# Kernel optimization log

Hardware: AMD Instinct MI355X
Metric: run time of the kernel (lower is better)

## Reference

```python
import jax, jax.numpy as jnp
import numpy as np

N_FACTORS = 4
N_ITERATIONS = 2
N_LAYERS = 1
DEG_EPS = 1e-8
L2_EPS = 1e-12


def _l2norm(x):
    # torch F.normalize(p=2, dim=1): x / max(||x||, eps)
    n = jnp.sqrt(jnp.sum(x * x, axis=-1, keepdims=True))
    return x / jnp.maximum(n, L2_EPS)


def setup_inputs() -> dict:
    key = jax.random.key(0)
    k1, k2, k3, k4, k5, k6, k7 = jax.random.split(key, 7)
    n_users, n_items, D, M, B = 40000, 20000, 128, 600000, 4096
    return {
        "user_emb": jax.random.normal(k1, (n_users, D), dtype=jnp.float32) * 0.02,
        "item_emb": jax.random.normal(k2, (n_items, D), dtype=jnp.float32) * 0.02,
        "row": jax.random.randint(k3, (M,), 0, n_users, dtype=jnp.int32),
        "col": jax.random.randint(k4, (M,), 0, n_items, dtype=jnp.int32),
        "users": jax.random.randint(k5, (B,), 0, n_users, dtype=jnp.int32),
        "pos": jax.random.randint(k6, (B,), 0, n_items, dtype=jnp.int32),
        "neg": jax.random.randint(k7, (B,), 0, n_items, dtype=jnp.int32),
    }


def reference(user_emb, item_emb, row, col, users, pos, neg):
    n_users = user_emb.shape[0]
    n_nodes = n_users + item_emb.shape[0]
    D = user_emb.shape[1]
    d = D // N_FACTORS

    # symmetric edge list: (u -> i+offset) and (i+offset -> u)
    h = jnp.concatenate([row, col + n_users])  # [E]
    t = jnp.concatenate([col + n_users, row])  # [E]
    E = h.shape[0]

    ego = jnp.concatenate([user_emb, item_emb], axis=0)  # [N, D]
    A = jnp.ones((E, N_FACTORS), dtype=ego.dtype)
    all_emb = [ego]

    for _layer in range(N_LAYERS):
        ego_f = ego.reshape(n_nodes, N_FACTORS, d)  # factor chunks
        factor_emb = None
        for it in range(N_ITERATIONS):
            # build_matrix: per-factor edge softmax + D^-0.5 A D^-0.5
            norm_A = jax.nn.softmax(A, axis=1)                         # [E, F]
            deg = jax.ops.segment_sum(norm_A, h, num_segments=n_nodes)  # [N, F]
            deg = 1.0 / jnp.sqrt(jnp.maximum(deg, DEG_EPS))
            edge_w = norm_A * deg[h] * deg[t]                          # [E, F]
            # per-factor sparse spmm: gather tail, weight, scatter to head
            edge_val = ego_f[t] * edge_w[:, :, None]                   # [E, F, d]
            factor_emb = jax.ops.segment_sum(edge_val, h, num_segments=n_nodes)  # [N, F, d]
            if it < N_ITERATIONS - 1:
                # routing score update (final update is unused by forward)
                hn = _l2norm(factor_emb[h])   # [E, F, d]
                tn = _l2norm(ego_f[t])        # [E, F, d]
                A = A + jnp.sum(hn * jnp.tanh(tn), axis=-1)
        ego = factor_emb.reshape(n_nodes, D)
        all_emb.append(ego)

    out = jnp.mean(jnp.stack(all_emb, axis=1), axis=1)  # [N, D]
    u_g = out[:n_users]
    i_g = out[n_users:]
    return u_g[users], i_g[pos], i_g[neg]
```

## Files before the change

### kernel.cpp

```cpp
#include <hip/hip_runtime.h>
#include <hip/hip_fp16.h>
#include <math.h>

#define NU 40000
#define NI 20000
#define NN 60000
#define DD 128
#define NF 4
#define ME 600000
#define NE 1200000
#define NB 4096
#define NBLK 235
#define CPAD 16


__device__ __forceinline__ const float* node_row(const float* ue, const float* ie, int n) {
    return (n < NU) ? (ue + (size_t)n * DD) : (ie + (size_t)(n - NU) * DD);
}

typedef _Float16 hf2_t __attribute__((ext_vector_type(2)));
__device__ __forceinline__ float fdot2f(unsigned int a, unsigned int b, float c) {
#if __has_builtin(__builtin_amdgcn_fdot2)
    return __builtin_amdgcn_fdot2(__builtin_bit_cast(hf2_t, a),
                                  __builtin_bit_cast(hf2_t, b), c, false);
#else
    float2 fa = __half22float2(__builtin_bit_cast(__half2, a));
    float2 fb = __half22float2(__builtin_bit_cast(__half2, b));
    return c + fa.x * fb.x + fa.y * fb.y;
#endif
}


__global__ void k_zero(int* counts, unsigned char* flags) {
    int i = blockIdx.x * blockDim.x + threadIdx.x;
    if (i < NN * CPAD) counts[i] = 0;
    if (i < NN) flags[i] = 0;
}

__global__ void k_flag(const int* __restrict__ users, const int* __restrict__ pos,
                       const int* __restrict__ neg, unsigned char* __restrict__ flags) {
    int i = blockIdx.x * blockDim.x + threadIdx.x;
    if (i >= 3 * NB) return;
    int which = i >> 12, k = i & 4095;
    int n = (which == 0) ? users[k] : ((which == 1) ? NU + pos[k] : NU + neg[k]);
    flags[n] = 1;
}

__global__ void k_count(const int* __restrict__ row, const int* __restrict__ col,
                        int* __restrict__ counts, int* __restrict__ rank) {
    int base = (blockIdx.x * blockDim.x + threadIdx.x) * 4;
    if (base >= NE) return;
    int4 h4;
    if (base < ME) {
        h4 = *(const int4*)(row + base);
    } else {
        int4 c4 = *(const int4*)(col + (base - ME));
        h4 = make_int4(NU + c4.x, NU + c4.y, NU + c4.z, NU + c4.w);
    }
    int4 r;
    r.x = atomicAdd(&counts[h4.x * CPAD], 1);
    r.y = atomicAdd(&counts[h4.y * CPAD], 1);
    r.z = atomicAdd(&counts[h4.z * CPAD], 1);
    r.w = atomicAdd(&counts[h4.w * CPAD], 1);
    *(int4*)(rank + base) = r;
}


__global__ void k_scanA(const int* __restrict__ counts, int* __restrict__ pre,
                        int* __restrict__ bsum) {
    int tid = threadIdx.x;
    int i = blockIdx.x * 256 + tid;
    int v = (i < NN) ? counts[i * CPAD] : 0;
    int lane = tid & 63, w = tid >> 6;
    int s = v;
    #pragma unroll
    for (int off = 1; off < 64; off <<= 1) {
        int o = __shfl_up(s, off);
        if (lane >= off) s += o;
    }
    __shared__ int wsum[4];
    if (lane == 63) wsum[w] = s;
    __syncthreads();
    int add = 0;
    #pragma unroll
    for (int k = 0; k < 4; ++k) add += (k < w) ? wsum[k] : 0;
    if (i < NN) pre[i] = s - v + add;
    if (tid == 255) bsum[blockIdx.x] = add + s;
}

__global__ void k_scanB(const int* __restrict__ bsum, int* __restrict__ boff) {
    int tid = threadIdx.x;
    int v = (tid < NBLK) ? bsum[tid] : 0;
    int lane = tid & 63, w = tid >> 6;
    int s = v;
    #pragma unroll
    for (int off = 1; off < 64; off <<= 1) {
        int o = __shfl_up(s, off);
        if (lane >= off) s += o;
    }
    __shared__ int wsum[4];
    if (lane == 63) wsum[w] = s;
    __syncthreads();
    int add = 0;
    #pragma unroll
    for (int k = 0; k < 4; ++k) add += (k < w) ? wsum[k] : 0;
    if (tid < NBLK) boff[tid] = s - v + add;
}

__global__ void k_scanC(const int* __restrict__ pre, const int* __restrict__ boff,
                        const int* __restrict__ counts,
                        int* __restrict__ row_ptr, float* __restrict__ dinv0) {
    int i = blockIdx.x * 256 + threadIdx.x;
    if (i < NN) {
        row_ptr[i] = pre[i] + boff[blockIdx.x];
        dinv0[i]   = 1.0f / sqrtf(fmaxf(0.25f * (float)counts[i * CPAD], 1e-8f));
    }
    if (i == 0) row_ptr[NN] = NE;
}

__global__ void k_fill(const int* __restrict__ row, const int* __restrict__ col,
                       const int* __restrict__ row_ptr, const int* __restrict__ rank,
                       unsigned short* __restrict__ t_sorted) {
    int base = (blockIdx.x * blockDim.x + threadIdx.x) * 4;
    if (base >= NE) return;
    int4 h4, t4;
    if (base < ME) {
        h4 = *(const int4*)(row + base);
        int4 c4 = *(const int4*)(col + base);
        t4 = make_int4(NU + c4.x, NU + c4.y, NU + c4.z, NU + c4.w);
    } else {
        int4 c4 = *(const int4*)(col + (base - ME));
        h4 = make_int4(NU + c4.x, NU + c4.y, NU + c4.z, NU + c4.w);
        t4 = *(const int4*)(row + (base - ME));
    }
    int4 r = *(const int4*)(rank + base);
    t_sorted[row_ptr[h4.x] + r.x] = (unsigned short)t4.x;
    t_sorted[row_ptr[h4.y] + r.y] = (unsigned short)t4.y;
    t_sorted[row_ptr[h4.z] + r.z] = (unsigned short)t4.z;
    t_sorted[row_ptr[h4.w] + r.w] = (unsigned short)t4.w;
}

__global__ void k_prep(const float* __restrict__ ue, const float* __restrict__ ie,
                       const float* __restrict__ dinv0,
                       __half* __restrict__ ego16s, __half* __restrict__ ttan) {
    int i = blockIdx.x * blockDim.x + threadIdx.x;
    if (i >= NN * 16) return;
    int n = i >> 4;
    int il = i & 15;
    const float* src = node_row(ue, ie, n) + il * 8;
    float4 a = *(const float4*)src;
    float4 b = *(const float4*)(src + 4);
    float w = dinv0[n];
    __half2 h[4] = { __floats2half2_rn(w * a.x, w * a.y), __floats2half2_rn(w * a.z, w * a.w),
                     __floats2half2_rn(w * b.x, w * b.y), __floats2half2_rn(w * b.z, w * b.w) };
    ((float4*)ego16s)[i] = *(float4*)h;
    float s2 = a.x * a.x + a.y * a.y + a.z * a.z + a.w * a.w
             + b.x * b.x + b.y * b.y + b.z * b.z + b.w * b.w;
    s2 += __shfl_xor(s2, 1); s2 += __shfl_xor(s2, 2);
    float inv = 1.0f / fmaxf(sqrtf(s2), 1e-12f);
    __half2 t[4] = { __floats2half2_rn(tanhf(a.x * inv), tanhf(a.y * inv)),
                     __floats2half2_rn(tanhf(a.z * inv), tanhf(a.w * inv)),
                     __floats2half2_rn(tanhf(b.x * inv), tanhf(b.y * inv)),
                     __floats2half2_rn(tanhf(b.z * inv), tanhf(b.w * inv)) };
    ((float4*)ttan)[i] = *(float4*)t;
}

__global__ void k_mega(const int* __restrict__ row_ptr,
                       const unsigned short* __restrict__ t_sorted,
                       const __half* __restrict__ ego16s, const __half* __restrict__ ttan,
                       const unsigned char* __restrict__ flags,
                       float* __restrict__ normA, float* __restrict__ dinv1) {
    int n = blockIdx.x * 4 + (threadIdx.x >> 6);
    if (n >= NN) return;
    int lane = threadIdx.x & 63;
    int p0 = row_ptr[n], p1 = row_ptr[n + 1];
    bool writeA = flags[n] != 0;

    int g2 = lane >> 5;
    int jl = lane & 31;
    float4 acc = make_float4(0.f, 0.f, 0.f, 0.f);
    #pragma unroll 4
    for (int pb = p0; pb < p1; pb += 2) {
        int p = pb + g2;
        bool valid = p < p1;
        int pc = valid ? p : (p1 - 1);
        float m = valid ? 1.0f : 0.0f;
        int t = t_sorted[pc];
        float2 raw = ((const float2*)(ego16s + (size_t)t * DD))[jl];
        float2 v01 = __half22float2(*(const __half2*)&raw.x);
        float2 v23 = __half22float2(*(const __half2*)&raw.y);
        acc.x += m * v01.x; acc.y += m * v01.y;
        acc.z += m * v23.x; acc.w += m * v23.y;
    }
    acc.x += __shfl_xor(acc.x, 32); acc.y += __shfl_xor(acc.y, 32);
    acc.z += __shfl_xor(acc.z, 32); acc.w += __shfl_xor(acc.w, 32);
    float ss = acc.x * acc.x + acc.y * acc.y + acc.z * acc.z + acc.w * acc.w;
    ss += __shfl_xor(ss, 1); ss += __shfl_xor(ss, 2); ss += __shfl_xor(ss, 4);
    float inv = 1.0f / fmaxf(sqrtf(ss), 1e-12f);
    unsigned int u01 = __builtin_bit_cast(unsigned int,
                         __floats2half2_rn(acc.x * inv, acc.y * inv));
    unsigned int u23 = __builtin_bit_cast(unsigned int,
                         __floats2half2_rn(acc.z * inv, acc.w * inv));
    int il = lane & 15;
    uint4 au;
    au.x = __shfl(u01, 2 * il);
    au.y = __shfl(u23, 2 * il);
    au.z = __shfl(u01, 2 * il + 1);
    au.w = __shfl(u23, 2 * il + 1);

    int g = lane >> 4;
    int f = il >> 2;
    float dacc = 0.0f;
    #pragma unroll 4
    for (int pb = p0; pb < p1; pb += 4) {
        int p = pb + g;
        bool valid = p < p1;
        int pc = valid ? p : (p1 - 1);
        int t = t_sorted[pc];
        uint4 bu = ((const uint4*)(ttan + (size_t)t * DD))[il];
        float s = 0.0f;
        s = fdot2f(au.x, bu.x, s);
        s = fdot2f(au.y, bu.y, s);
        s = fdot2f(au.z, bu.z, s);
        s = fdot2f(au.w, bu.w, s);
        s += __shfl_xor(s, 1);
        s += __shfl_xor(s, 2);
        float m1 = fmaxf(s, __shfl_xor(s, 4));
        float mx = fmaxf(m1, __shfl_xor(m1, 8));
        float e = __expf(s - mx);
        float sum = e;
        sum += __shfl_xor(sum, 4);
        sum += __shfl_xor(sum, 8);
        float v = e * __builtin_amdgcn_rcpf(sum);
        if (valid) {
            if (writeA && (il & 3) == 0) normA[(size_t)pc * 4 + f] = v;
            dacc += v;
        }
    }
    dacc += __shfl_xor(dacc, 16);
    dacc += __shfl_xor(dacc, 32);
    if (g == 0 && (il & 3) == 0)
        dinv1[(size_t)n * 4 + f] = 1.0f / sqrtf(fmaxf(dacc, 1e-8f));
}

__global__ void k_prop1_out(const float* __restrict__ ue, const float* __restrict__ ie,
                            const int* __restrict__ row_ptr,
                            const unsigned short* __restrict__ t_sorted,
                            const float* __restrict__ normA, const float* __restrict__ dinv1,
                            const int* __restrict__ users, const int* __restrict__ pos,
                            const int* __restrict__ neg, float* __restrict__ out) {
    int r = blockIdx.x * 8 + (threadIdx.x >> 5);
    if (r >= 3 * NB) return;
    int j = threadIdx.x & 31;
    int f = j >> 3;
    int which = r >> 12;
    int i = r & 4095;
    int n;
    if (which == 0)      n = users[i];
    else if (which == 1) n = NU + pos[i];
    else                 n = NU + neg[i];
    int p0 = row_ptr[n], p1 = row_ptr[n + 1];
    float4 acc = make_float4(0.f, 0.f, 0.f, 0.f);
    #pragma unroll 4
    for (int p = p0; p < p1; ++p) {
        int t = t_sorted[p];
        float w = normA[(size_t)p * 4 + f] * dinv1[(size_t)t * 4 + f];
        float4 v = ((const float4*)node_row(ue, ie, t))[j];
        acc.x += w * v.x; acc.y += w * v.y;
        acc.z += w * v.z; acc.w += w * v.w;
    }
    float dn = dinv1[(size_t)n * 4 + f];
    float4 e0 = ((const float4*)node_row(ue, ie, n))[j];
    ((float4*)(out + (size_t)r * DD))[j] =
        make_float4(0.5f * (e0.x + dn * acc.x), 0.5f * (e0.y + dn * acc.y),
                    0.5f * (e0.z + dn * acc.z), 0.5f * (e0.w + dn * acc.w));
}


extern "C" void kernel_launch(void* const* d_in, const int* in_sizes, int n_in,
                              void* d_out, int out_size, void* d_ws, size_t ws_size,
                              hipStream_t stream) {
    const float* ue   = (const float*)d_in[0];
    const float* ie   = (const float*)d_in[1];
    const int* row    = (const int*)d_in[2];
    const int* col    = (const int*)d_in[3];
    const int* users  = (const int*)d_in[4];
    const int* pos    = (const int*)d_in[5];
    const int* neg    = (const int*)d_in[6];
    float* out        = (float*)d_out;

    char* ws = (char*)d_ws;
    size_t off = 0;
    auto take = [&](size_t bytes) { void* p = ws + off; off += (bytes + 255) & ~(size_t)255; return p; };
    __half* ttan     = (__half*)take((size_t)NN * DD * 2);
    __half* ego16s   = (__half*)take((size_t)NN * DD * 2);
    float*  normA    = (float*)take((size_t)NE * 4 * 4);
    float*  dinv1    = (float*)take((size_t)NN * 4 * 4);
    float*  dinv0    = (float*)take((size_t)NN * 4);
    int*    row_ptr  = (int*)take((size_t)(NN + 1) * 4);
    int*    counts   = (int*)take((size_t)NN * CPAD * 4);
    int*    pre      = (int*)take((size_t)NN * 4);
    int*    bsum     = (int*)take((size_t)NBLK * 4);
    int*    boff     = (int*)take((size_t)NBLK * 4);
    int*    rank     = (int*)take((size_t)NE * 4);
    unsigned short* t_sorted = (unsigned short*)take((size_t)NE * 2);
    unsigned char*  flags    = (unsigned char*)take((size_t)NN);
    if (off > ws_size) return;

    k_zero <<<(NN * CPAD + 255) / 256, 256, 0, stream>>>(counts, flags);
    k_flag <<<(3 * NB + 255) / 256, 256, 0, stream>>>(users, pos, neg, flags);
    k_count<<<(NE / 4 + 255) / 256, 256, 0, stream>>>(row, col, counts, rank);
    k_scanA<<<NBLK, 256, 0, stream>>>(counts, pre, bsum);
    k_scanB<<<1, 256, 0, stream>>>(bsum, boff);
    k_scanC<<<NBLK, 256, 0, stream>>>(pre, boff, counts, row_ptr, dinv0);
    k_prep <<<(NN * 16 + 255) / 256, 256, 0, stream>>>(ue, ie, dinv0, ego16s, ttan);
    k_fill <<<(NE / 4 + 255) / 256, 256, 0, stream>>>(row, col, row_ptr, rank, t_sorted);
    k_mega <<<(NN + 3) / 4, 256, 0, stream>>>(row_ptr, t_sorted, ego16s, ttan,
                                              flags, normA, (float*)dinv1);
    k_prop1_out<<<(3 * NB) / 8, 256, 0, stream>>>(ue, ie, row_ptr, t_sorted,
                                                  normA, (const float*)dinv1,
                                                  users, pos, neg, out);
}
```

Baseline: 277.4 us.

## Shrink rank and normA to 16-bit, process edge pairs jointly, reuse fp16 ego in final pass

Result: no change. 277.0 us (-0.1%).

```diff
diff --git a/kernel.cpp b/kernel.cpp
--- a/kernel.cpp
+++ b/kernel.cpp
@@ -30,6 +30,10 @@
 #endif
 }
 
+__device__ __forceinline__ unsigned int packh2(float a, float b) {
+    return __builtin_bit_cast(unsigned int, __floats2half2_rn(a, b));
+}
+
 
 __global__ void k_zero(int* counts, unsigned char* flags) {
     int i = blockIdx.x * blockDim.x + threadIdx.x;
@@ -47,22 +51,23 @@
 }
 
 __global__ void k_count(const int* __restrict__ row, const int* __restrict__ col,
-                        int* __restrict__ counts, int* __restrict__ rank) {
+                        int* __restrict__ counts, unsigned short* __restrict__ rank) {
     int base = (blockIdx.x * blockDim.x + threadIdx.x) * 4;
-    if (base >= NE) return;
-    int4 h4;
-    if (base < ME) {
-        h4 = *(const int4*)(row + base);
-    } else {
-        int4 c4 = *(const int4*)(col + (base - ME));
-        h4 = make_int4(NU + c4.x, NU + c4.y, NU + c4.z, NU + c4.w);
-    }
-    int4 r;
-    r.x = atomicAdd(&counts[h4.x * CPAD], 1);
-    r.y = atomicAdd(&counts[h4.y * CPAD], 1);
-    r.z = atomicAdd(&counts[h4.z * CPAD], 1);
-    r.w = atomicAdd(&counts[h4.w * CPAD], 1);
-    *(int4*)(rank + base) = r;
+    if (base >= ME) return;
+    int4 r4 = *(const int4*)(row + base);
+    int4 c4 = *(const int4*)(col + base);
+    unsigned int f0 = atomicAdd(&counts[r4.x * CPAD], 1);
+    unsigned int v0 = atomicAdd(&counts[(NU + c4.x) * CPAD], 1);
+    unsigned int f1 = atomicAdd(&counts[r4.y * CPAD], 1);
+    unsigned int v1 = atomicAdd(&counts[(NU + c4.y) * CPAD], 1);
+    unsigned int f2 = atomicAdd(&counts[r4.z * CPAD], 1);
+    unsigned int v2 = atomicAdd(&counts[(NU + c4.z) * CPAD], 1);
+    unsigned int f3 = atomicAdd(&counts[r4.w * CPAD], 1);
+    unsigned int v3 = atomicAdd(&counts[(NU + c4.w) * CPAD], 1);
+    uint2 fw = make_uint2(f0 | (f1 << 16), f2 | (f3 << 16));
+    uint2 rv = make_uint2(v0 | (v1 << 16), v2 | (v3 << 16));
+    *(uint2*)(rank + base)      = fw;
+    *(uint2*)(rank + ME + base) = rv;
 }
 
 
@@ -108,36 +113,36 @@
 }
 
 __global__ void k_scanC(const int* __restrict__ pre, const int* __restrict__ boff,
-                        const int* __restrict__ counts,
-                        int* __restrict__ row_ptr, float* __restrict__ dinv0) {
+                        const int* __restrict__ counts, int* __restrict__ row_ptr,
+                        float* __restrict__ dinv0, float* __restrict__ inv0) {
     int i = blockIdx.x * 256 + threadIdx.x;
     if (i < NN) {
         row_ptr[i] = pre[i] + boff[blockIdx.x];
-        dinv0[i]   = 1.0f / sqrtf(fmaxf(0.25f * (float)counts[i * CPAD], 1e-8f));
+        float d = sqrtf(fmaxf(0.25f * (float)counts[i * CPAD], 1e-8f));
+        dinv0[i] = 1.0f / d;
+        inv0[i]  = d;
     }
     if (i == 0) row_ptr[NN] = NE;
 }
 
 __global__ void k_fill(const int* __restrict__ row, const int* __restrict__ col,
-                       const int* __restrict__ row_ptr, const int* __restrict__ rank,
+                       const int* __restrict__ row_ptr,
+                       const unsigned short* __restrict__ rank,
                        unsigned short* __restrict__ t_sorted) {
     int base = (blockIdx.x * blockDim.x + threadIdx.x) * 4;
-    if (base >= NE) return;
-    int4 h4, t4;
-    if (base < ME) {
-        h4 = *(const int4*)(row + base);
-        int4 c4 = *(const int4*)(col + base);
-        t4 = make_int4(NU + c4.x, NU + c4.y, NU + c4.z, NU + c4.w);
-    } else {
-        int4 c4 = *(const int4*)(col + (base - ME));
-        h4 = make_int4(NU + c4.x, NU + c4.y, NU + c4.z, NU + c4.w);
-        t4 = *(const int4*)(row + (base - ME));
-    }
-    int4 r = *(const int4*)(rank + base);
-    t_sorted[row_ptr[h4.x] + r.x] = (unsigned short)t4.x;
-    t_sorted[row_ptr[h4.y] + r.y] = (unsigned short)t4.y;
-    t_sorted[row_ptr[h4.z] + r.z] = (unsigned short)t4.z;
-    t_sorted[row_ptr[h4.w] + r.w] = (unsigned short)t4.w;
+    if (base >= ME) return;
+    int4 r4 = *(const int4*)(row + base);
+    int4 c4 = *(const int4*)(col + base);
+    uint2 fw = *(const uint2*)(rank + base);
+    uint2 rv = *(const uint2*)(rank + ME + base);
+    t_sorted[row_ptr[r4.x]      + (fw.x & 0xffff)] = (unsigned short)(NU + c4.x);
+    t_sorted[row_ptr[r4.y]      + (fw.x >> 16)]    = (unsigned short)(NU + c4.y);
+    t_sorted[row_ptr[r4.z]      + (fw.y & 0xffff)] = (unsigned short)(NU + c4.z);
+    t_sorted[row_ptr[r4.w]      + (fw.y >> 16)]    = (unsigned short)(NU + c4.w);
+    t_sorted[row_ptr[NU + c4.x] + (rv.x & 0xffff)] = (unsigned short)r4.x;
+    t_sorted[row_ptr[NU + c4.y] + (rv.x >> 16)]    = (unsigned short)r4.y;
+    t_sorted[row_ptr[NU + c4.z] + (rv.y & 0xffff)] = (unsigned short)r4.z;
+    t_sorted[row_ptr[NU + c4.w] + (rv.y >> 16)]    = (unsigned short)r4.w;
 }
 
 __global__ void k_prep(const float* __restrict__ ue, const float* __restrict__ ie,
@@ -169,71 +174,71 @@
                        const unsigned short* __restrict__ t_sorted,
                        const __half* __restrict__ ego16s, const __half* __restrict__ ttan,
                        const unsigned char* __restrict__ flags,
-                       float* __restrict__ normA, float* __restrict__ dinv1) {
+                       __half* __restrict__ normA, float* __restrict__ dinv1) {
     int n = blockIdx.x * 4 + (threadIdx.x >> 6);
     if (n >= NN) return;
     int lane = threadIdx.x & 63;
+    int g  = lane >> 4;
+    int il = lane & 15;
+    int f  = il >> 2;
     int p0 = row_ptr[n], p1 = row_ptr[n + 1];
     bool writeA = flags[n] != 0;
 
-    int g2 = lane >> 5;
-    int jl = lane & 31;
-    float4 acc = make_float4(0.f, 0.f, 0.f, 0.f);
-    #pragma unroll 4
-    for (int pb = p0; pb < p1; pb += 2) {
-        int p = pb + g2;
-        bool valid = p < p1;
-        int pc = valid ? p : (p1 - 1);
-        float m = valid ? 1.0f : 0.0f;
-        int t = t_sorted[pc];
-        float2 raw = ((const float2*)(ego16s + (size_t)t * DD))[jl];
-        float2 v01 = __half22float2(*(const __half2*)&raw.x);
-        float2 v23 = __half22float2(*(const __half2*)&raw.y);
-        acc.x += m * v01.x; acc.y += m * v01.y;
-        acc.z += m * v23.x; acc.w += m * v23.y;
-    }
-    acc.x += __shfl_xor(acc.x, 32); acc.y += __shfl_xor(acc.y, 32);
-    acc.z += __shfl_xor(acc.z, 32); acc.w += __shfl_xor(acc.w, 32);
-    float ss = acc.x * acc.x + acc.y * acc.y + acc.z * acc.z + acc.w * acc.w;
-    ss += __shfl_xor(ss, 1); ss += __shfl_xor(ss, 2); ss += __shfl_xor(ss, 4);
+    float4 acA = make_float4(0.f, 0.f, 0.f, 0.f);
+    float4 acB = make_float4(0.f, 0.f, 0.f, 0.f);
+    #pragma unroll 2
+    for (int pb = p0; pb < p1; pb += 4) {
+        int p = pb + g;
+        if (p < p1) {
+            int t = t_sorted[p];
+            uint4 raw = ((const uint4*)(ego16s + (size_t)t * DD))[il];
+            float2 v0 = __half22float2(__builtin_bit_cast(__half2, raw.x));
+            float2 v1 = __half22float2(__builtin_bit_cast(__half2, raw.y));
+            float2 v2 = __half22float2(__builtin_bit_cast(__half2, raw.z));
+            float2 v3 = __half22float2(__builtin_bit_cast(__half2, raw.w));
+            acA.x += v0.x; acA.y += v0.y; acA.z += v1.x; acA.w += v1.y;
+            acB.x += v2.x; acB.y += v2.y; acB.z += v3.x; acB.w += v3.y;
+        }
+    }
+    acA.x += __shfl_xor(acA.x, 16); acA.x += __shfl_xor(acA.x, 32);
+    acA.y += __shfl_xor(acA.y, 16); acA.y += __shfl_xor(acA.y, 32);
+    acA.z += __shfl_xor(acA.z, 16); acA.z += __shfl_xor(acA.z, 32);
+    acA.w += __shfl_xor(acA.w, 16); acA.w += __shfl_xor(acA.w, 32);
+    acB.x += __shfl_xor(acB.x, 16); acB.x += __shfl_xor(acB.x, 32);
+    acB.y += __shfl_xor(acB.y, 16); acB.y += __shfl_xor(acB.y, 32);
+    acB.z += __shfl_xor(acB.z, 16); acB.z += __shfl_xor(acB.z, 32);
+    acB.w += __shfl_xor(acB.w, 16); acB.w += __shfl_xor(acB.w, 32);
+    float ss = acA.x * acA.x + acA.y * acA.y + acA.z * acA.z + acA.w * acA.w
+             + acB.x * acB.x + acB.y * acB.y + acB.z * acB.z + acB.w * acB.w;
+    ss += __shfl_xor(ss, 1); ss += __shfl_xor(ss, 2);
     float inv = 1.0f / fmaxf(sqrtf(ss), 1e-12f);
-    unsigned int u01 = __builtin_bit_cast(unsigned int,
-                         __floats2half2_rn(acc.x * inv, acc.y * inv));
-    unsigned int u23 = __builtin_bit_cast(unsigned int,
-                         __floats2half2_rn(acc.z * inv, acc.w * inv));
-    int il = lane & 15;
-    uint4 au;
-    au.x = __shfl(u01, 2 * il);
-    au.y = __shfl(u23, 2 * il);
-    au.z = __shfl(u01, 2 * il + 1);
-    au.w = __shfl(u23, 2 * il + 1);
-
-    int g = lane >> 4;
-    int f = il >> 2;
+    uint4 au = make_uint4(packh2(acA.x * inv, acA.y * inv),
+                          packh2(acA.z * inv, acA.w * inv),
+                          packh2(acB.x * inv, acB.y * inv),
+                          packh2(acB.z * inv, acB.w * inv));
+
     float dacc = 0.0f;
     #pragma unroll 4
     for (int pb = p0; pb < p1; pb += 4) {
         int p = pb + g;
-        bool valid = p < p1;
-        int pc = valid ? p : (p1 - 1);
-        int t = t_sorted[pc];
-        uint4 bu = ((const uint4*)(ttan + (size_t)t * DD))[il];
-        float s = 0.0f;
-        s = fdot2f(au.x, bu.x, s);
-        s = fdot2f(au.y, bu.y, s);
-        s = fdot2f(au.z, bu.z, s);
-        s = fdot2f(au.w, bu.w, s);
-        s += __shfl_xor(s, 1);
-        s += __shfl_xor(s, 2);
-        float m1 = fmaxf(s, __shfl_xor(s, 4));
-        float mx = fmaxf(m1, __shfl_xor(m1, 8));
-        float e = __expf(s - mx);
-        float sum = e;
-        sum += __shfl_xor(sum, 4);
-        sum += __shfl_xor(sum, 8);
-        float v = e * __builtin_amdgcn_rcpf(sum);
-        if (valid) {
-            if (writeA && (il & 3) == 0) normA[(size_t)pc * 4 + f] = v;
+        if (p < p1) {
+            int t = t_sorted[p];
+            uint4 bu = ((const uint4*)(ttan + (size_t)t * DD))[il];
+            float s = 0.0f;
+            s = fdot2f(au.x, bu.x, s);
+            s = fdot2f(au.y, bu.y, s);
+            s = fdot2f(au.z, bu.z, s);
+            s = fdot2f(au.w, bu.w, s);
+            s += __shfl_xor(s, 1);
+            s += __shfl_xor(s, 2);
+            float m1 = fmaxf(s, __shfl_xor(s, 4));
+            float mx = fmaxf(m1, __shfl_xor(m1, 8));
+            float e = __expf(s - mx);
+            float sum = e;
+            sum += __shfl_xor(sum, 4);
+            sum += __shfl_xor(sum, 8);
+            float v = e * __builtin_amdgcn_rcpf(sum);
+            if (writeA && (il & 3) == 0) normA[(size_t)p * 4 + f] = __float2half(v);
             dacc += v;
         }
     }
@@ -244,9 +249,11 @@
 }
 
 __global__ void k_prop1_out(const float* __restrict__ ue, const float* __restrict__ ie,
+                            const __half* __restrict__ ego16s,
+                            const float* __restrict__ inv0,
                             const int* __restrict__ row_ptr,
                             const unsigned short* __restrict__ t_sorted,
-                            const float* __restrict__ normA, const float* __restrict__ dinv1,
+                            const __half* __restrict__ normA, const float* __restrict__ dinv1,
                             const int* __restrict__ users, const int* __restrict__ pos,
                             const int* __restrict__ neg, float* __restrict__ out) {
     int r = blockIdx.x * 8 + (threadIdx.x >> 5);
@@ -264,10 +271,13 @@
     #pragma unroll 4
     for (int p = p0; p < p1; ++p) {
         int t = t_sorted[p];
-        float w = normA[(size_t)p * 4 + f] * dinv1[(size_t)t * 4 + f];
-        float4 v = ((const float4*)node_row(ue, ie, t))[j];
-        acc.x += w * v.x; acc.y += w * v.y;
-        acc.z += w * v.z; acc.w += w * v.w;
+        float w = __half2float(normA[(size_t)p * 4 + f])
+                * dinv1[(size_t)t * 4 + f] * inv0[t];
+        float2 raw = ((const float2*)(ego16s + (size_t)t * DD))[j];
+        float2 v01 = __half22float2(*(const __half2*)&raw.x);
+        float2 v23 = __half22float2(*(const __half2*)&raw.y);
+        acc.x += w * v01.x; acc.y += w * v01.y;
+        acc.z += w * v23.x; acc.w += w * v23.y;
     }
     float dn = dinv1[(size_t)n * 4 + f];
     float4 e0 = ((const float4*)node_row(ue, ie, n))[j];
@@ -294,30 +304,31 @@
     auto take = [&](size_t bytes) { void* p = ws + off; off += (bytes + 255) & ~(size_t)255; return p; };
     __half* ttan     = (__half*)take((size_t)NN * DD * 2);
     __half* ego16s   = (__half*)take((size_t)NN * DD * 2);
-    float*  normA    = (float*)take((size_t)NE * 4 * 4);
+    __half* normA    = (__half*)take((size_t)NE * 4 * 2);
     float*  dinv1    = (float*)take((size_t)NN * 4 * 4);
     float*  dinv0    = (float*)take((size_t)NN * 4);
+    float*  inv0     = (float*)take((size_t)NN * 4);
     int*    row_ptr  = (int*)take((size_t)(NN + 1) * 4);
     int*    counts   = (int*)take((size_t)NN * CPAD * 4);
     int*    pre      = (int*)take((size_t)NN * 4);
     int*    bsum     = (int*)take((size_t)NBLK * 4);
     int*    boff     = (int*)take((size_t)NBLK * 4);
-    int*    rank     = (int*)take((size_t)NE * 4);
+    unsigned short* rank     = (unsigned short*)take((size_t)NE * 2);
     unsigned short* t_sorted = (unsigned short*)take((size_t)NE * 2);
     unsigned char*  flags    = (unsigned char*)take((size_t)NN);
     if (off > ws_size) return;
 
     k_zero <<<(NN * CPAD + 255) / 256, 256, 0, stream>>>(counts, flags);
     k_flag <<<(3 * NB + 255) / 256, 256, 0, stream>>>(users, pos, neg, flags);
-    k_count<<<(NE / 4 + 255) / 256, 256, 0, stream>>>(row, col, counts, rank);
+    k_count<<<(ME / 4 + 255) / 256, 256, 0, stream>>>(row, col, counts, rank);
     k_scanA<<<NBLK, 256, 0, stream>>>(counts, pre, bsum);
     k_scanB<<<1, 256, 0, stream>>>(bsum, boff);
-    k_scanC<<<NBLK, 256, 0, stream>>>(pre, boff, counts, row_ptr, dinv0);
+    k_scanC<<<NBLK, 256, 0, stream>>>(pre, boff, counts, row_ptr, dinv0, inv0);
     k_prep <<<(NN * 16 + 255) / 256, 256, 0, stream>>>(ue, ie, dinv0, ego16s, ttan);
-    k_fill <<<(NE / 4 + 255) / 256, 256, 0, stream>>>(row, col, row_ptr, rank, t_sorted);
+    k_fill <<<(ME / 4 + 255) / 256, 256, 0, stream>>>(row, col, row_ptr, rank, t_sorted);
     k_mega <<<(NN + 3) / 4, 256, 0, stream>>>(row_ptr, t_sorted, ego16s, ttan,
                                               flags, normA, (float*)dinv1);
-    k_prop1_out<<<(3 * NB) / 8, 256, 0, stream>>>(ue, ie, row_ptr, t_sorted,
-                                                  normA, (const float*)dinv1,
+    k_prop1_out<<<(3 * NB) / 8, 256, 0, stream>>>(ue, ie, ego16s, inv0, row_ptr,
+                                                  t_sorted, normA, (const float*)dinv1,
                                                   users, pos, neg, out);
 }
```
